# Kernel optimization log

Measured on AMD Instinct MI355X. Metric: run time of the kernel, lower is better.

The kernel has to match this reference:

```python
import jax, jax.numpy as jnp
import numpy as np
from jax import lax

START_IDX = 0
STOP_IDX = 1


def _forward_alg(feats_lbt, mask_lb, transitions):
    # feats_lbt: [L, B, T], mask_lb: [L, B], transitions[i, j] = score(j -> i)
    L, B, T = feats_lbt.shape
    init = jnp.full((B, T), -10000.0, dtype=feats_lbt.dtype).at[:, START_IDX].set(0.0)

    def step(fv, xs):
        feat, m = xs  # feat: [B, T], m: [B]
        # scores[b, next, prev] = fv[b, prev] + transitions[next, prev] + feat[b, next]
        scores = fv[:, None, :] + transitions[None, :, :] + feat[:, :, None]
        alphas = jax.nn.logsumexp(scores, axis=-1)  # [B, T]
        fv = jnp.where(m[:, None] > 0, alphas, fv)
        return fv, None

    fv, _ = lax.scan(step, init, (feats_lbt, mask_lb))
    terminal = fv + transitions[STOP_IDX][None, :]
    return jax.nn.logsumexp(terminal, axis=-1)  # [B]


def _score_sentence(feats_lbt, tags_bl, mask_lb, transitions):
    L, B, T = feats_lbt.shape
    start_col = jnp.full((B, 1), START_IDX, dtype=tags_bl.dtype)
    tags_ext = jnp.concatenate([start_col, tags_bl], axis=-1)  # [B, L+1]
    # transition scores along the gold path: [B, L]
    trans = transitions[tags_ext[:, 1:], tags_ext[:, :-1]]
    # emission scores: feats is [L, B, T] -> gather per-position gold tag
    emit = jnp.take_along_axis(
        feats_lbt, tags_bl.T[:, :, None], axis=-1
    )[:, :, 0]  # [L, B]
    step_scores = (trans.T + emit) * (mask_lb > 0)  # [L, B]
    score = step_scores.sum(axis=0)  # [B]
    lengths = mask_lb.sum(axis=0).astype(jnp.int32)  # [B]
    last_tag = tags_ext[jnp.arange(B), lengths]
    score = score + transitions[STOP_IDX, last_tag]
    return score


def setup_inputs() -> dict:
    key = jax.random.key(0)
    k1, k2, k3 = jax.random.split(key, 3)
    B, L, T = 256, 2048, 32
    efeats = jax.random.normal(k1, (B, L, T), dtype=jnp.float32)
    mask = jnp.ones((B, L), dtype=jnp.float32)
    tgt = jax.random.randint(k2, (B, L), 0, T, dtype=jnp.int32)
    transitions = jax.random.normal(k3, (T, T), dtype=jnp.float32)
    return {"efeats": efeats, "mask": mask, "tgt": tgt, "transitions": transitions}


def reference(efeats, mask, tgt, transitions):
    B, L = mask.shape
    mask_lb = mask.T  # [L, B]
    feats_lbt = jnp.transpose(efeats, (1, 0, 2))  # [L, B, T]
    forward_score = _forward_alg(feats_lbt, mask_lb, transitions)
    gold_score = _score_sentence(feats_lbt, tgt, mask_lb, transitions)
    loss = (forward_score - gold_score).sum() / B
    return loss
```

## Files before the change

### kernel.cpp

```cpp
#include <hip/hip_runtime.h>

#define B_SZ 256
#define L_SZ 2048
#define T_SZ 32
#define START_IDX 0
#define STOP_IDX 1

#define CLEN 64
#define NCHB 8
#define NCH_SEQ 32
#define NBLK_SEQ 4
#define NCHUNK_TOT (B_SZ * NCH_SEQ)

#define FB_NCH 16
#define FB_CLEN 128

typedef __attribute__((ext_vector_type(8))) short bf16x8;
typedef __attribute__((ext_vector_type(4))) float f32x4;

__device__ __forceinline__ unsigned fau(float f){ union{float f; unsigned u;} v; v.f=f; return v.u; }
__device__ __forceinline__ float uaf(unsigned u){ union{unsigned u; float f;} v; v.u=u; return v.f; }
__device__ __forceinline__ int pack_trunc(float lo, float hi){
  return (int)__builtin_amdgcn_perm(fau(hi), fau(lo), 0x07060302u);
}
__device__ __forceinline__ bf16x8 frag_of(const int* p){
  union{ int i[4]; bf16x8 v; } u;
  u.i[0]=p[0]; u.i[1]=p[1]; u.i[2]=p[2]; u.i[3]=p[3];
  return u.v;
}

__global__ void zero_kernel(float* out){ if(threadIdx.x==0) out[0]=0.f; }

__global__ __launch_bounds__(512, 8) void crf_chunk_kernel(
    const float* __restrict__ efeats, const float* __restrict__ mask,
    const int* __restrict__ tgt, const float* __restrict__ trans,
    unsigned short* __restrict__ wsM, int* __restrict__ wsE,
    float* __restrict__ wsG, float* __restrict__ wsL)
{
  __shared__ float s_trans[T_SZ*T_SZ];
  __shared__ float s_d[NCHB][128];

  const int tid  = threadIdx.x;
  const int w    = tid >> 6;
  const int lane = tid & 63;
  const int g    = lane >> 4;
  const int c16  = lane & 15;

  const int b  = blockIdx.x >> 2;
  const int q  = blockIdx.x & 3;
  const int c  = q*NCHB + w;
  const int l0 = c * CLEN;

  s_trans[tid]     = trans[tid];
  s_trans[tid+512] = trans[tid+512];
  __syncthreads();

  int a0[4], a1[4];
  #pragma unroll
  for (int I=0; I<2; ++I){
    int row = 8*(c16>>2) + 4*I + (c16&3);
    float e[8];
    #pragma unroll
    for (int j=0;j<8;++j) e[j] = __expf(s_trans[row*T_SZ + 8*g + j]);
    int* dst = I ? a1 : a0;
    #pragma unroll
    for (int p=0;p<4;++p) dst[p] = pack_trunc(e[2*p], e[2*p+1]);
  }

  int b0[4], b1[4];
  #pragma unroll
  for (int p=0;p<4;++p){
    int s0 = 8*g + 2*p, s1 = s0+1;
    unsigned lo = (s0==c16)?0x3f80u:0u, hi = (s1==c16)?0x3f80u:0u;
    b0[p] = (int)(lo | (hi<<16));
    lo = (s0==16+c16)?0x3f80u:0u; hi = (s1==16+c16)?0x3f80u:0u;
    b1[p] = (int)(lo | (hi<<16));
  }

  const long fbase = ((long)b * L_SZ) * T_SZ;
  const int  mbase = b*L_SZ + l0;

  float maskv = mask[mbase + lane];
  int   tcur  = tgt [mbase + lane];
  int   tprev;
  {
    int lp = (l0 + lane == 0) ? mbase : (mbase + lane - 1);
    tprev = tgt[lp];
    if (l0 + lane == 0) tprev = START_IDX;
  }

  float emitg = efeats[fbase + (long)(l0+lane)*T_SZ + tcur];
  float gl = (maskv > 0.f) ? (s_trans[tcur*T_SZ + tprev] + emitg) : 0.f;
  float ml = maskv;
  #pragma unroll
  for (int off=32; off>0; off>>=1){ gl += __shfl_xor(gl, off, 64); ml += __shfl_xor(ml, off, 64); }

  unsigned long long mbits = __ballot(maskv > 0.f);

  const float* fpt = efeats + fbase + (long)l0*T_SZ;
  float f0raw = fpt[lane];
  float fq[4];
  #pragma unroll
  for (int i=1; i<=4; ++i) fq[i&3] = fpt[i*64 + lane];
  s_d[w][lane] = __expf(f0raw);

  int esum = 0;
  const f32x4 zf = {0.f,0.f,0.f,0.f};

  #pragma unroll 4
  for (int p=0; p<32; ++p){
    if (p < 31){
      s_d[w][((p+1)&1)*64 + lane] = __expf(fq[(p+1)&3]);
      int np = p+5; if (np > 31) np = 31;
      fq[(p+1)&3] = fpt[np*64 + lane];
    }
    const float* dbase = &s_d[w][(p&1)*64];
    #pragma unroll
    for (int h=0; h<2; ++h){
      int t = 2*p + h;
      if ((mbits >> t) & 1ull){
        f32x4 c00 = __builtin_amdgcn_mfma_f32_16x16x32_bf16(frag_of(a0), frag_of(b0), zf, 0,0,0);
        f32x4 c01 = __builtin_amdgcn_mfma_f32_16x16x32_bf16(frag_of(a0), frag_of(b1), zf, 0,0,0);
        f32x4 c10 = __builtin_amdgcn_mfma_f32_16x16x32_bf16(frag_of(a1), frag_of(b0), zf, 0,0,0);
        f32x4 c11 = __builtin_amdgcn_mfma_f32_16x16x32_bf16(frag_of(a1), frag_of(b1), zf, 0,0,0);

        const float4* dv = (const float4*)(dbase + h*32);
        float4 dl = dv[2*g], dh = dv[2*g+1];
        float f0=dl.x, f1=dl.y, f2=dl.z, f3=dl.w;
        float f4=dh.x, f5=dh.y, f6=dh.z, f7=dh.w;

        if (h==1 && (p&1)==1){
          float m00 = c00[0]*f0;
          unsigned mb2 = (unsigned)__builtin_amdgcn_readfirstlane((int)fau(m00));
          int e = (int)((mb2>>23)&255u) - 127;
          esum += e;
          float r = uaf((unsigned)(127-e)<<23);
          f0*=r; f1*=r; f2*=r; f3*=r; f4*=r; f5*=r; f6*=r; f7*=r;
        }

        c00[0]*=f0; c00[1]*=f1; c00[2]*=f2; c00[3]*=f3;
        c01[0]*=f0; c01[1]*=f1; c01[2]*=f2; c01[3]*=f3;
        c10[0]*=f4; c10[1]*=f5; c10[2]*=f6; c10[3]*=f7;
        c11[0]*=f4; c11[1]*=f5; c11[2]*=f6; c11[3]*=f7;

        b0[0]=pack_trunc(c00[0],c00[1]); b0[1]=pack_trunc(c00[2],c00[3]);
        b0[2]=pack_trunc(c10[0],c10[1]); b0[3]=pack_trunc(c10[2],c10[3]);
        b1[0]=pack_trunc(c01[0],c01[1]); b1[1]=pack_trunc(c01[2],c01[3]);
        b1[2]=pack_trunc(c11[0],c11[1]); b1[3]=pack_trunc(c11[2],c11[3]);
      }
    }
  }

  unsigned short* Mptr = wsM + (long)(b*NCH_SEQ + c) * (T_SZ*T_SZ);
  #pragma unroll
  for (int pp=0; pp<4; ++pp){
    int s = 8*g + 2*pp;
    *(int*)((char*)Mptr + ((c16*T_SZ + s)*2))        = b0[pp];
    *(int*)((char*)Mptr + (((16+c16)*T_SZ + s)*2))   = b1[pp];
  }
  if (lane==0){
    int cg = b*NCH_SEQ + c;
    wsE[cg]=esum; wsG[cg]=gl; wsL[cg]=ml;
  }
}

__global__ __launch_bounds__(256) void crf_combine_kernel(
    const unsigned short* __restrict__ wsM, const int* __restrict__ wsE,
    const float* __restrict__ wsG, const float* __restrict__ wsL,
    const int* __restrict__ tgt, const float* __restrict__ trans,
    float* __restrict__ out)
{
  __shared__ unsigned short sM[NCH_SEQ*T_SZ*T_SZ];
  __shared__ int   s_es[NCH_SEQ];
  __shared__ float s_g[NCH_SEQ], s_ml[NCH_SEQ];

  const int tid = threadIdx.x;
  const int b   = blockIdx.x;

  const uint4* src = (const uint4*)(wsM + (long)b*NCH_SEQ*T_SZ*T_SZ);
  uint4* dst = (uint4*)sM;
  #pragma unroll
  for (int i=0;i<16;++i) dst[tid + i*256] = src[tid + i*256];
  if (tid < NCH_SEQ){
    s_es[tid]=wsE[b*NCH_SEQ+tid]; s_g[tid]=wsG[b*NCH_SEQ+tid]; s_ml[tid]=wsL[b*NCH_SEQ+tid];
  }
  __syncthreads();

  if (tid < 64){
    int s = tid & 31;
    float v = (s==START_IDX)?1.f:0.f;
    int E = 0;
    for (int cc=0; cc<NCH_SEQ; ++cc){
      const unsigned short* M = &sM[cc*T_SZ*T_SZ];
      float u = 0.f;
      #pragma unroll 8
      for (int k=0;k<T_SZ;++k){
        float mv = uaf(((unsigned)M[k*T_SZ + s])<<16);
        float vk = uaf((unsigned)__builtin_amdgcn_readlane((int)fau(v), k));
        u = fmaf(mv, vk, u);
      }
      unsigned ub = (unsigned)__builtin_amdgcn_readfirstlane((int)fau(u));
      int eu = (int)((ub>>23)&255u)-127;
      E += s_es[cc] + eu;
      v = u * uaf((unsigned)(127-eu)<<23);
    }
    float term = v * __expf(trans[STOP_IDX*T_SZ + s]);
    #pragma unroll
    for (int off=16; off>0; off>>=1) term += __shfl_xor(term, off, 32);
    float fwd = (float)E * 0.69314718055994530942f + __logf(term);

    float gp = s_g[s];
    float lp = s_ml[s];
    #pragma unroll
    for (int off=16; off>0; off>>=1){ gp += __shfl_xor(gp, off, 32); lp += __shfl_xor(lp, off, 32); }
    int len = (int)lp;
    int last_tag = (len==0)? START_IDX : tgt[b*L_SZ + len-1];
    float goldT = gp + trans[STOP_IDX*T_SZ + last_tag];
    if (tid==0) atomicAdd(out, (fwd - goldT) * (1.0f/B_SZ));
  }
}

__global__ __launch_bounds__(1024) void crf_loss_kernel(
    const float* __restrict__ efeats, const float* __restrict__ mask,
    const int* __restrict__ tgt, const float* __restrict__ trans,
    float* __restrict__ out)
{
  __shared__ float s_trans[T_SZ*T_SZ];
  __shared__ float s_d[FB_NCH][T_SZ];
  __shared__ unsigned short s_M[FB_NCH][T_SZ*T_SZ];
  __shared__ int   s_es[FB_NCH];
  __shared__ float s_gd[FB_NCH];
  __shared__ float s_mlv[FB_NCH];

  const int tid  = threadIdx.x;
  const int b    = blockIdx.x;
  const int w    = tid >> 6;
  const int lane = tid & 63;
  const int g    = lane >> 4;
  const int c16  = lane & 15;
  const int i32  = lane & 31;

  s_trans[tid] = trans[tid];
  __syncthreads();

  int a0[4], a1[4];
  #pragma unroll
  for (int I=0; I<2; ++I){
    int row = 8*(c16>>2) + 4*I + (c16&3);
    float e[8];
    #pragma unroll
    for (int j=0;j<8;++j) e[j] = __expf(s_trans[row*T_SZ + 8*g + j]);
    int* dst = I ? a1 : a0;
    #pragma unroll
    for (int p=0;p<4;++p) dst[p] = pack_trunc(e[2*p], e[2*p+1]);
  }

  int b0[4], b1[4];
  #pragma unroll
  for (int p=0;p<4;++p){
    int s0 = 8*g + 2*p, s1 = s0+1;
    unsigned lo = (s0==c16)?0x3f80u:0u, hi = (s1==c16)?0x3f80u:0u;
    b0[p] = (int)(lo | (hi<<16));
    lo = (s0==16+c16)?0x3f80u:0u; hi = (s1==16+c16)?0x3f80u:0u;
    b1[p] = (int)(lo | (hi<<16));
  }

  const int l0 = w * FB_CLEN;
  const long fbase = ((long)b * L_SZ) * T_SZ;

  float fqv[4];
  #pragma unroll
  for (int i=0;i<4;++i) fqv[i] = efeats[fbase + (long)(l0+i)*T_SZ + i32];

  int   tA = tgt [b*L_SZ + l0 + lane];
  int   tB = tgt [b*L_SZ + l0 + 64 + lane];
  float mA = mask[b*L_SZ + l0 + lane];
  float mB = mask[b*L_SZ + l0 + 64 + lane];
  int prev = (l0==0) ? START_IDX : tgt[b*L_SZ + l0 - 1];

  int esum = 0;
  float gold = 0.f, mlen = 0.f;
  const f32x4 zf = {0.f,0.f,0.f,0.f};

  #pragma unroll 4
  for (int t=0; t<FB_CLEN; ++t){
    float fcur = fqv[t&3];
    int lpf = l0 + t + 4; lpf = (lpf < L_SZ) ? lpf : (L_SZ-1);
    fqv[t&3] = efeats[fbase + (long)lpf*T_SZ + i32];

    float mk  = uaf((unsigned)__builtin_amdgcn_readlane((int)fau((t<64)?mA:mB), t&63));
    int   cur = __builtin_amdgcn_readlane((t<64)?tA:tB, t&63);
    mlen += mk;

    if (mk > 0.f){
      if (lane < 32) s_d[w][lane] = __expf(fcur);

      f32x4 c00 = __builtin_amdgcn_mfma_f32_16x16x32_bf16(frag_of(a0), frag_of(b0), zf, 0,0,0);
      f32x4 c01 = __builtin_amdgcn_mfma_f32_16x16x32_bf16(frag_of(a0), frag_of(b1), zf, 0,0,0);
      f32x4 c10 = __builtin_amdgcn_mfma_f32_16x16x32_bf16(frag_of(a1), frag_of(b0), zf, 0,0,0);
      f32x4 c11 = __builtin_amdgcn_mfma_f32_16x16x32_bf16(frag_of(a1), frag_of(b1), zf, 0,0,0);

      const float4* dv = (const float4*)(&s_d[w][0]);
      float4 dl = dv[2*g], dh = dv[2*g+1];
      float f0=dl.x, f1=dl.y, f2=dl.z, f3=dl.w;
      float f4=dh.x, f5=dh.y, f6=dh.z, f7=dh.w;

      float m00 = c00[0]*f0;
      unsigned mb = (unsigned)__builtin_amdgcn_readfirstlane((int)fau(m00));
      int e = (int)((mb>>23)&255u) - 127;
      esum += e;
      float r = uaf((unsigned)(127-e)<<23);
      f0*=r; f1*=r; f2*=r; f3*=r; f4*=r; f5*=r; f6*=r; f7*=r;

      c00[0]*=f0; c00[1]*=f1; c00[2]*=f2; c00[3]*=f3;
      c01[0]*=f0; c01[1]*=f1; c01[2]*=f2; c01[3]*=f3;
      c10[0]*=f4; c10[1]*=f5; c10[2]*=f6; c10[3]*=f7;
      c11[0]*=f4; c11[1]*=f5; c11[2]*=f6; c11[3]*=f7;

      b0[0]=pack_trunc(c00[0],c00[1]); b0[1]=pack_trunc(c00[2],c00[3]);
      b0[2]=pack_trunc(c10[0],c10[1]); b0[3]=pack_trunc(c10[2],c10[3]);
      b1[0]=pack_trunc(c01[0],c01[1]); b1[1]=pack_trunc(c01[2],c01[3]);
      b1[2]=pack_trunc(c11[0],c11[1]); b1[3]=pack_trunc(c11[2],c11[3]);

      float tp   = s_trans[cur*T_SZ + prev];
      float emit = uaf((unsigned)__builtin_amdgcn_readlane((int)fau(fcur), cur));
      gold += tp + emit;
    }
    prev = cur;
  }

  #pragma unroll
  for (int p=0;p<4;++p){
    int s = 8*g + 2*p;
    *(int*)((char*)(&s_M[w][0]) + (((long)(c16   )*T_SZ + s) * 2)) = b0[p];
    *(int*)((char*)(&s_M[w][0]) + (((long)(16+c16)*T_SZ + s) * 2)) = b1[p];
  }
  if (lane==0){ s_es[w]=esum; s_gd[w]=gold; s_mlv[w]=mlen; }
  __syncthreads();

  if (w==0){
    int s = i32;
    float v = (s==START_IDX)?1.f:0.f;
    int E = 0;
    for (int c=0;c<FB_NCH;++c){
      float u=0.f;
      #pragma unroll 8
      for (int k=0;k<T_SZ;++k){
        float mv = uaf(((unsigned)s_M[c][k*T_SZ + s])<<16);
        float vk = uaf((unsigned)__builtin_amdgcn_readlane((int)fau(v), k));
        u = fmaf(mv, vk, u);
      }
      unsigned ub = (unsigned)__builtin_amdgcn_readfirstlane((int)fau(u));
      int eu = (int)((ub>>23)&255u)-127;
      E += s_es[c] + eu;
      v = u * uaf((unsigned)(127-eu)<<23);
    }
    float term = v * __expf(s_trans[STOP_IDX*T_SZ + s]);
    #pragma unroll
    for (int off=16; off>0; off>>=1) term += __shfl_xor(term, off, 32);
    float fwd = (float)E * 0.69314718055994530942f + __logf(term);

    float gp = (s<FB_NCH)? s_gd[s] : 0.f;
    float lp = (s<FB_NCH)? s_mlv[s] : 0.f;
    #pragma unroll
    for (int off=16; off>0; off>>=1){ gp += __shfl_xor(gp, off, 32); lp += __shfl_xor(lp, off, 32); }
    int len = (int)lp;
    int last_tag = (len==0)? START_IDX : tgt[b*L_SZ + (len-1)];
    float goldT = gp + s_trans[STOP_IDX*T_SZ + last_tag];
    if (tid==0) atomicAdd(out, (fwd - goldT) * (1.0f/B_SZ));
  }
}

extern "C" void kernel_launch(void* const* d_in, const int* in_sizes, int n_in,
                              void* d_out, int out_size, void* d_ws, size_t ws_size,
                              hipStream_t stream)
{
  const float* efeats = (const float*)d_in[0];
  const float* mask   = (const float*)d_in[1];
  const int*   tgt    = (const int*)d_in[2];
  const float* trans  = (const float*)d_in[3];
  float* out = (float*)d_out;

  const size_t needM = (size_t)NCHUNK_TOT * T_SZ * T_SZ * 2;
  const size_t need  = needM + (size_t)NCHUNK_TOT * 12;

  zero_kernel<<<dim3(1), dim3(64), 0, stream>>>(out);

  if (ws_size >= need){
    unsigned short* wsM = (unsigned short*)d_ws;
    char* p = (char*)d_ws + needM;
    int*   wsE = (int*)p;
    float* wsG = (float*)(p + (size_t)NCHUNK_TOT*4);
    float* wsL = (float*)(p + (size_t)NCHUNK_TOT*8);
    crf_chunk_kernel<<<dim3(B_SZ*NBLK_SEQ), dim3(512), 0, stream>>>(
        efeats, mask, tgt, trans, wsM, wsE, wsG, wsL);
    crf_combine_kernel<<<dim3(B_SZ), dim3(256), 0, stream>>>(
        wsM, wsE, wsG, wsL, tgt, trans, out);
  } else {
    crf_loss_kernel<<<dim3(B_SZ), dim3(1024), 0, stream>>>(efeats, mask, tgt, trans, out);
  }
}
```

Measured before the change: 153.2 us.

## Tree-reduce chunk transfer matrices in-block via MFMA, shrink combine pass

Each block now multiplies its 8 per-wave chunk transfer matrices together in shared memory with a 3-level MFMA tree reduction, writing one matrix per block instead of 8 per block to the workspace. The combine kernel then chains only 4 matrices per sequence with 64 threads instead of 32 matrix-vector steps with 256 threads. The chunk loop also gains an all-mask-set fast path using packed 2-wide float multiplies, and occupancy bounds drop from 8 to 6. This trades extra in-block matrix products, barriers and shared memory for less workspace traffic and a shorter serial combine, with extra bf16 rounding from the intermediate products.

```diff
diff --git a/kernel.cpp b/kernel.cpp
--- a/kernel.cpp
+++ b/kernel.cpp
@@ -10,13 +10,14 @@
 #define NCHB 8
 #define NCH_SEQ 32
 #define NBLK_SEQ 4
-#define NCHUNK_TOT (B_SZ * NCH_SEQ)
+#define NBLK_TOT (B_SZ * NBLK_SEQ)
 
 #define FB_NCH 16
 #define FB_CLEN 128
 
 typedef __attribute__((ext_vector_type(8))) short bf16x8;
 typedef __attribute__((ext_vector_type(4))) float f32x4;
+typedef __attribute__((ext_vector_type(2))) float f32x2;
 
 __device__ __forceinline__ unsigned fau(float f){ union{float f; unsigned u;} v; v.f=f; return v.u; }
 __device__ __forceinline__ float uaf(unsigned u){ union{unsigned u; float f;} v; v.u=u; return v.f; }
@@ -31,7 +32,50 @@
 
 __global__ void zero_kernel(float* out){ if(threadIdx.x==0) out[0]=0.f; }
 
-__global__ __launch_bounds__(512, 8) void crf_chunk_kernel(
+__device__ __forceinline__ int mat_prod(const unsigned short* L, const unsigned short* Rt,
+                                        unsigned short* dst, bool writeT, int lane)
+{
+  const int g = lane >> 4, c16 = lane & 15;
+  const int ko = 8*g;
+  bf16x8 A0 = *(const bf16x8*)(L  + (c16*T_SZ      + ko));
+  bf16x8 A1 = *(const bf16x8*)(L  + ((16+c16)*T_SZ + ko));
+  bf16x8 B0 = *(const bf16x8*)(Rt + (c16*T_SZ      + ko));
+  bf16x8 B1 = *(const bf16x8*)(Rt + ((16+c16)*T_SZ + ko));
+  const f32x4 zf = {0.f,0.f,0.f,0.f};
+  f32x4 q00 = __builtin_amdgcn_mfma_f32_16x16x32_bf16(A0, B0, zf, 0,0,0);
+  f32x4 q01 = __builtin_amdgcn_mfma_f32_16x16x32_bf16(A0, B1, zf, 0,0,0);
+  f32x4 q10 = __builtin_amdgcn_mfma_f32_16x16x32_bf16(A1, B0, zf, 0,0,0);
+  f32x4 q11 = __builtin_amdgcn_mfma_f32_16x16x32_bf16(A1, B1, zf, 0,0,0);
+
+  unsigned mb = (unsigned)__builtin_amdgcn_readfirstlane((int)fau(q00[0]));
+  int e = (int)((mb>>23)&255u) - 127;
+  float r = uaf((unsigned)(127-e)<<23);
+  #pragma unroll
+  for (int i=0;i<4;++i){ q00[i]*=r; q01[i]*=r; q10[i]*=r; q11[i]*=r; }
+
+  if (!writeT){
+    #pragma unroll
+    for (int reg=0; reg<4; ++reg){
+      int x0 = 4*g + reg, x1 = 16 + 4*g + reg;
+      dst[x0*T_SZ + c16]      = (unsigned short)(fau(q00[reg])>>16);
+      dst[x0*T_SZ + 16 + c16] = (unsigned short)(fau(q01[reg])>>16);
+      dst[x1*T_SZ + c16]      = (unsigned short)(fau(q10[reg])>>16);
+      dst[x1*T_SZ + 16 + c16] = (unsigned short)(fau(q11[reg])>>16);
+    }
+  } else {
+    #pragma unroll
+    for (int rp=0; rp<2; ++rp){
+      int xb0 = 4*g + 2*rp, xb1 = 16 + 4*g + 2*rp;
+      *(int*)&dst[c16*T_SZ + xb0]        = pack_trunc(q00[2*rp], q00[2*rp+1]);
+      *(int*)&dst[(16+c16)*T_SZ + xb0]   = pack_trunc(q01[2*rp], q01[2*rp+1]);
+      *(int*)&dst[c16*T_SZ + xb1]        = pack_trunc(q10[2*rp], q10[2*rp+1]);
+      *(int*)&dst[(16+c16)*T_SZ + xb1]   = pack_trunc(q11[2*rp], q11[2*rp+1]);
+    }
+  }
+  return e;
+}
+
+__global__ __launch_bounds__(512, 6) void crf_chunk_kernel(
     const float* __restrict__ efeats, const float* __restrict__ mask,
     const int* __restrict__ tgt, const float* __restrict__ trans,
     unsigned short* __restrict__ wsM, int* __restrict__ wsE,
@@ -39,6 +83,9 @@
 {
   __shared__ float s_trans[T_SZ*T_SZ];
   __shared__ float s_d[NCHB][128];
+  __shared__ unsigned short s_tree[NCHB][T_SZ*T_SZ];
+  __shared__ int   s_et[NCHB];
+  __shared__ float s_gd[NCHB], s_ml[NCHB];
 
   const int tid  = threadIdx.x;
   const int w    = tid >> 6;
@@ -107,116 +154,195 @@
   int esum = 0;
   const f32x4 zf = {0.f,0.f,0.f,0.f};
 
-  #pragma unroll 4
-  for (int p=0; p<32; ++p){
-    if (p < 31){
+  if (mbits == ~0ull){
+    #pragma unroll 2
+    for (int p=0; p<32; ++p){
       s_d[w][((p+1)&1)*64 + lane] = __expf(fq[(p+1)&3]);
-      int np = p+5; if (np > 31) np = 31;
+      int np = p+5; np = (np>31)?31:np;
       fq[(p+1)&3] = fpt[np*64 + lane];
-    }
-    const float* dbase = &s_d[w][(p&1)*64];
-    #pragma unroll
-    for (int h=0; h<2; ++h){
-      int t = 2*p + h;
-      if ((mbits >> t) & 1ull){
+      const float* dbase = &s_d[w][(p&1)*64];
+      #pragma unroll
+      for (int h=0; h<2; ++h){
         f32x4 c00 = __builtin_amdgcn_mfma_f32_16x16x32_bf16(frag_of(a0), frag_of(b0), zf, 0,0,0);
         f32x4 c01 = __builtin_amdgcn_mfma_f32_16x16x32_bf16(frag_of(a0), frag_of(b1), zf, 0,0,0);
         f32x4 c10 = __builtin_amdgcn_mfma_f32_16x16x32_bf16(frag_of(a1), frag_of(b0), zf, 0,0,0);
         f32x4 c11 = __builtin_amdgcn_mfma_f32_16x16x32_bf16(frag_of(a1), frag_of(b1), zf, 0,0,0);
 
         const float4* dv = (const float4*)(dbase + h*32);
-        float4 dl = dv[2*g], dh = dv[2*g+1];
-        float f0=dl.x, f1=dl.y, f2=dl.z, f3=dl.w;
-        float f4=dh.x, f5=dh.y, f6=dh.z, f7=dh.w;
+        float4 dl = dv[2*g], dh2 = dv[2*g+1];
+        f32x2 d01 = {dl.x, dl.y}, d23 = {dl.z, dl.w};
+        f32x2 d45 = {dh2.x, dh2.y}, d67 = {dh2.z, dh2.w};
 
         if (h==1 && (p&1)==1){
-          float m00 = c00[0]*f0;
+          float m00 = c00[0]*d01[0];
           unsigned mb2 = (unsigned)__builtin_amdgcn_readfirstlane((int)fau(m00));
           int e = (int)((mb2>>23)&255u) - 127;
           esum += e;
-          float r = uaf((unsigned)(127-e)<<23);
-          f0*=r; f1*=r; f2*=r; f3*=r; f4*=r; f5*=r; f6*=r; f7*=r;
+          float rr = uaf((unsigned)(127-e)<<23);
+          f32x2 rv = {rr, rr};
+          d01 *= rv; d23 *= rv; d45 *= rv; d67 *= rv;
         }
 
-        c00[0]*=f0; c00[1]*=f1; c00[2]*=f2; c00[3]*=f3;
-        c01[0]*=f0; c01[1]*=f1; c01[2]*=f2; c01[3]*=f3;
-        c10[0]*=f4; c10[1]*=f5; c10[2]*=f6; c10[3]*=f7;
-        c11[0]*=f4; c11[1]*=f5; c11[2]*=f6; c11[3]*=f7;
-
-        b0[0]=pack_trunc(c00[0],c00[1]); b0[1]=pack_trunc(c00[2],c00[3]);
-        b0[2]=pack_trunc(c10[0],c10[1]); b0[3]=pack_trunc(c10[2],c10[3]);
-        b1[0]=pack_trunc(c01[0],c01[1]); b1[1]=pack_trunc(c01[2],c01[3]);
-        b1[2]=pack_trunc(c11[0],c11[1]); b1[3]=pack_trunc(c11[2],c11[3]);
+        f32x2 p00 = {c00[0],c00[1]}; p00 *= d01;
+        f32x2 p01 = {c00[2],c00[3]}; p01 *= d23;
+        f32x2 p10 = {c01[0],c01[1]}; p10 *= d01;
+        f32x2 p11 = {c01[2],c01[3]}; p11 *= d23;
+        f32x2 p20 = {c10[0],c10[1]}; p20 *= d45;
+        f32x2 p21 = {c10[2],c10[3]}; p21 *= d67;
+        f32x2 p30 = {c11[0],c11[1]}; p30 *= d45;
+        f32x2 p31 = {c11[2],c11[3]}; p31 *= d67;
+
+        b0[0]=pack_trunc(p00[0],p00[1]); b0[1]=pack_trunc(p01[0],p01[1]);
+        b0[2]=pack_trunc(p20[0],p20[1]); b0[3]=pack_trunc(p21[0],p21[1]);
+        b1[0]=pack_trunc(p10[0],p10[1]); b1[1]=pack_trunc(p11[0],p11[1]);
+        b1[2]=pack_trunc(p30[0],p30[1]); b1[3]=pack_trunc(p31[0],p31[1]);
       }
     }
-  }
-
-  unsigned short* Mptr = wsM + (long)(b*NCH_SEQ + c) * (T_SZ*T_SZ);
-  #pragma unroll
-  for (int pp=0; pp<4; ++pp){
-    int s = 8*g + 2*pp;
-    *(int*)((char*)Mptr + ((c16*T_SZ + s)*2))        = b0[pp];
-    *(int*)((char*)Mptr + (((16+c16)*T_SZ + s)*2))   = b1[pp];
-  }
-  if (lane==0){
-    int cg = b*NCH_SEQ + c;
-    wsE[cg]=esum; wsG[cg]=gl; wsL[cg]=ml;
-  }
-}
-
-__global__ __launch_bounds__(256) void crf_combine_kernel(
+  } else {
+    #pragma unroll 2
+    for (int p=0; p<32; ++p){
+      if (p < 31){
+        s_d[w][((p+1)&1)*64 + lane] = __expf(fq[(p+1)&3]);
+        int np = p+5; if (np > 31) np = 31;
+        fq[(p+1)&3] = fpt[np*64 + lane];
+      }
+      const float* dbase = &s_d[w][(p&1)*64];
+      #pragma unroll
+      for (int h=0; h<2; ++h){
+        int t = 2*p + h;
+        if ((mbits >> t) & 1ull){
+          f32x4 c00 = __builtin_amdgcn_mfma_f32_16x16x32_bf16(frag_of(a0), frag_of(b0), zf, 0,0,0);
+          f32x4 c01 = __builtin_amdgcn_mfma_f32_16x16x32_bf16(frag_of(a0), frag_of(b1), zf, 0,0,0);
+          f32x4 c10 = __builtin_amdgcn_mfma_f32_16x16x32_bf16(frag_of(a1), frag_of(b0), zf, 0,0,0);
+          f32x4 c11 = __builtin_amdgcn_mfma_f32_16x16x32_bf16(frag_of(a1), frag_of(b1), zf, 0,0,0);
+
+          const float4* dv = (const float4*)(dbase + h*32);
+          float4 dl = dv[2*g], dh2 = dv[2*g+1];
+          float f0=dl.x, f1=dl.y, f2=dl.z, f3=dl.w;
+          float f4=dh2.x, f5=dh2.y, f6=dh2.z, f7=dh2.w;
+
+          if (h==1 && (p&1)==1){
+            float m00 = c00[0]*f0;
+            unsigned mb2 = (unsigned)__builtin_amdgcn_readfirstlane((int)fau(m00));
+            int e = (int)((mb2>>23)&255u) - 127;
+            esum += e;
+            float rr = uaf((unsigned)(127-e)<<23);
+            f0*=rr; f1*=rr; f2*=rr; f3*=rr; f4*=rr; f5*=rr; f6*=rr; f7*=rr;
+          }
+
+          c00[0]*=f0; c00[1]*=f1; c00[2]*=f2; c00[3]*=f3;
+          c01[0]*=f0; c01[1]*=f1; c01[2]*=f2; c01[3]*=f3;
+          c10[0]*=f4; c10[1]*=f5; c10[2]*=f6; c10[3]*=f7;
+          c11[0]*=f4; c11[1]*=f5; c11[2]*=f6; c11[3]*=f7;
+
+          b0[0]=pack_trunc(c00[0],c00[1]); b0[1]=pack_trunc(c00[2],c00[3]);
+          b0[2]=pack_trunc(c10[0],c10[1]); b0[3]=pack_trunc(c10[2],c10[3]);
+          b1[0]=pack_trunc(c01[0],c01[1]); b1[1]=pack_trunc(c01[2],c01[3]);
+          b1[2]=pack_trunc(c11[0],c11[1]); b1[3]=pack_trunc(c11[2],c11[3]);
+        }
+      }
+    }
+  }
+
+  if ((w & 1) == 0){
+    unsigned short* R = &s_tree[w][0];
+    #pragma unroll
+    for (int p=0;p<4;++p){
+      int s = 8*g + 2*p;
+      *(int*)&R[c16*T_SZ + s]      = b0[p];
+      *(int*)&R[(16+c16)*T_SZ + s] = b1[p];
+    }
+  } else {
+    unsigned short* T = &s_tree[w][0];
+    #pragma unroll
+    for (int p=0;p<4;++p){
+      int s = 8*g + 2*p;
+      T[s*T_SZ + c16]           = (unsigned short)(b0[p] & 0xffff);
+      T[(s+1)*T_SZ + c16]       = (unsigned short)(((unsigned)b0[p])>>16);
+      T[s*T_SZ + 16 + c16]      = (unsigned short)(b1[p] & 0xffff);
+      T[(s+1)*T_SZ + 16 + c16]  = (unsigned short)(((unsigned)b1[p])>>16);
+    }
+  }
+  if (lane==0){ s_et[w]=esum; s_gd[w]=gl; s_ml[w]=ml; }
+  __syncthreads();
+
+  if (w < 4){
+    int e = mat_prod(&s_tree[2*w][0], &s_tree[2*w+1][0], &s_tree[2*w][0], (w&1)!=0, lane);
+    if (lane==0) s_et[2*w] = s_et[2*w] + s_et[2*w+1] + e;
+  }
+  __syncthreads();
+  if (w < 2){
+    int e = mat_prod(&s_tree[4*w][0], &s_tree[4*w+2][0], &s_tree[4*w][0], (w&1)!=0, lane);
+    if (lane==0) s_et[4*w] = s_et[4*w] + s_et[4*w+2] + e;
+  }
+  __syncthreads();
+  if (w == 0){
+    int e = mat_prod(&s_tree[0][0], &s_tree[4][0], &s_tree[0][0], false, lane);
+    if (lane==0) s_et[0] = s_et[0] + s_et[4] + e;
+  }
+  __syncthreads();
+
+  const int bid = blockIdx.x;
+  ((int*)(wsM + (long)bid*(T_SZ*T_SZ)))[tid] = ((const int*)&s_tree[0][0])[tid];
+  if (tid == 0){
+    wsE[bid] = s_et[0];
+    float gs=0.f, ls=0.f;
+    #pragma unroll
+    for (int i=0;i<NCHB;++i){ gs += s_gd[i]; ls += s_ml[i]; }
+    wsG[bid] = gs; wsL[bid] = ls;
+  }
+}
+
+__global__ __launch_bounds__(64) void crf_combine_kernel(
     const unsigned short* __restrict__ wsM, const int* __restrict__ wsE,
     const float* __restrict__ wsG, const float* __restrict__ wsL,
     const int* __restrict__ tgt, const float* __restrict__ trans,
     float* __restrict__ out)
 {
-  __shared__ unsigned short sM[NCH_SEQ*T_SZ*T_SZ];
-  __shared__ int   s_es[NCH_SEQ];
-  __shared__ float s_g[NCH_SEQ], s_ml[NCH_SEQ];
+  __shared__ unsigned short sM[NBLK_SEQ*T_SZ*T_SZ];
+  __shared__ float s_v[T_SZ];
 
   const int tid = threadIdx.x;
   const int b   = blockIdx.x;
 
-  const uint4* src = (const uint4*)(wsM + (long)b*NCH_SEQ*T_SZ*T_SZ);
-  uint4* dst = (uint4*)sM;
-  #pragma unroll
-  for (int i=0;i<16;++i) dst[tid + i*256] = src[tid + i*256];
-  if (tid < NCH_SEQ){
-    s_es[tid]=wsE[b*NCH_SEQ+tid]; s_g[tid]=wsG[b*NCH_SEQ+tid]; s_ml[tid]=wsL[b*NCH_SEQ+tid];
-  }
-  __syncthreads();
-
-  if (tid < 64){
-    int s = tid & 31;
-    float v = (s==START_IDX)?1.f:0.f;
-    int E = 0;
-    for (int cc=0; cc<NCH_SEQ; ++cc){
-      const unsigned short* M = &sM[cc*T_SZ*T_SZ];
-      float u = 0.f;
-      #pragma unroll 8
-      for (int k=0;k<T_SZ;++k){
-        float mv = uaf(((unsigned)M[k*T_SZ + s])<<16);
-        float vk = uaf((unsigned)__builtin_amdgcn_readlane((int)fau(v), k));
-        u = fmaf(mv, vk, u);
-      }
-      unsigned ub = (unsigned)__builtin_amdgcn_readfirstlane((int)fau(u));
-      int eu = (int)((ub>>23)&255u)-127;
-      E += s_es[cc] + eu;
-      v = u * uaf((unsigned)(127-eu)<<23);
-    }
-    float term = v * __expf(trans[STOP_IDX*T_SZ + s]);
-    #pragma unroll
-    for (int off=16; off>0; off>>=1) term += __shfl_xor(term, off, 32);
-    float fwd = (float)E * 0.69314718055994530942f + __logf(term);
-
-    float gp = s_g[s];
-    float lp = s_ml[s];
-    #pragma unroll
-    for (int off=16; off>0; off>>=1){ gp += __shfl_xor(gp, off, 32); lp += __shfl_xor(lp, off, 32); }
+  const uint4* src = (const uint4*)(wsM + (long)b*NBLK_SEQ*T_SZ*T_SZ);
+  #pragma unroll
+  for (int i=0;i<8;++i) ((uint4*)sM)[tid + i*64] = src[tid + i*64];
+  __syncthreads();
+
+  const int s = tid & 31;
+  float v = (s==START_IDX)?1.f:0.f;
+  int E = 0;
+  #pragma unroll
+  for (int j=0; j<NBLK_SEQ; ++j){
+    if (tid < 32) s_v[s] = v;
+    __syncthreads();
+    const unsigned short* M = &sM[j*T_SZ*T_SZ];
+    float u = 0.f;
+    #pragma unroll 8
+    for (int x=0; x<T_SZ; ++x){
+      float mv = uaf(((unsigned)M[x*T_SZ + s])<<16);
+      u = fmaf(mv, s_v[x], u);
+    }
+    unsigned ub = (unsigned)__builtin_amdgcn_readfirstlane((int)fau(u));
+    int eu = (int)((ub>>23)&255u)-127;
+    E += wsE[b*NBLK_SEQ + j] + eu;
+    v = u * uaf((unsigned)(127-eu)<<23);
+    __syncthreads();
+  }
+  float term = v * __expf(trans[STOP_IDX*T_SZ + s]);
+  #pragma unroll
+  for (int off=16; off>0; off>>=1) term += __shfl_xor(term, off, 32);
+  float fwd = (float)E * 0.69314718055994530942f + __logf(term);
+
+  if (tid == 0){
+    float gp = 0.f, lp = 0.f;
+    #pragma unroll
+    for (int j=0;j<NBLK_SEQ;++j){ gp += wsG[b*NBLK_SEQ+j]; lp += wsL[b*NBLK_SEQ+j]; }
     int len = (int)lp;
     int last_tag = (len==0)? START_IDX : tgt[b*L_SZ + len-1];
     float goldT = gp + trans[STOP_IDX*T_SZ + last_tag];
-    if (tid==0) atomicAdd(out, (fwd - goldT) * (1.0f/B_SZ));
+    atomicAdd(out, (fwd - goldT) * (1.0f/B_SZ));
   }
 }
 
@@ -381,8 +507,8 @@
   const float* trans  = (const float*)d_in[3];
   float* out = (float*)d_out;
 
-  const size_t needM = (size_t)NCHUNK_TOT * T_SZ * T_SZ * 2;
-  const size_t need  = needM + (size_t)NCHUNK_TOT * 12;
+  const size_t needM = (size_t)NBLK_TOT * T_SZ * T_SZ * 2;
+  const size_t need  = needM + (size_t)NBLK_TOT * 12;
 
   zero_kernel<<<dim3(1), dim3(64), 0, stream>>>(out);
 
@@ -390,11 +516,11 @@
     unsigned short* wsM = (unsigned short*)d_ws;
     char* p = (char*)d_ws + needM;
     int*   wsE = (int*)p;
-    float* wsG = (float*)(p + (size_t)NCHUNK_TOT*4);
-    float* wsL = (float*)(p + (size_t)NCHUNK_TOT*8);
-    crf_chunk_kernel<<<dim3(B_SZ*NBLK_SEQ), dim3(512), 0, stream>>>(
+    float* wsG = (float*)(p + (size_t)NBLK_TOT*4);
+    float* wsL = (float*)(p + (size_t)NBLK_TOT*8);
+    crf_chunk_kernel<<<dim3(NBLK_TOT), dim3(512), 0, stream>>>(
         efeats, mask, tgt, trans, wsM, wsE, wsG, wsL);
-    crf_combine_kernel<<<dim3(B_SZ), dim3(256), 0, stream>>>(
+    crf_combine_kernel<<<dim3(B_SZ), dim3(64), 0, stream>>>(
         wsM, wsE, wsG, wsL, tgt, trans, out);
   } else {
     crf_loss_kernel<<<dim3(B_SZ), dim3(1024), 0, stream>>>(efeats, mask, tgt, trans, out);
```

Measured after the change: 142.5 us. -7.0%, faster.
